# Optimization experiments

Hardware: AMD Instinct MI355X
Metric: run time of the kernel (lower is better)

The kernel has to match this reference:

```python
import jax, jax.numpy as jnp
import numpy as np

N_NODES = 50000
N_EDGES = 800000
DIM = 128
HEADS = 8
DK = DIM // HEADS  # 16
SQRT_DK = float(np.sqrt(DK))


def setup_inputs() -> dict:
    key = jax.random.key(0)
    ks = jax.random.split(key, 12)
    inp = {
        "h": jax.random.normal(ks[0], (N_NODES, DIM), jnp.float32),
        "src": jax.random.randint(ks[1], (N_EDGES,), 0, N_NODES, jnp.int32),
        "dst": jax.random.randint(ks[2], (N_EDGES,), 0, N_NODES, jnp.int32),
        "Wk": jax.random.normal(ks[3], (DIM, DIM), jnp.float32) / np.sqrt(DIM),
        "bk": jnp.zeros((DIM,), jnp.float32),
        "Wq": jax.random.normal(ks[4], (DIM, DIM), jnp.float32) / np.sqrt(DIM),
        "bq": jnp.zeros((DIM,), jnp.float32),
        "Wv": jax.random.normal(ks[5], (DIM, DIM), jnp.float32) / np.sqrt(DIM),
        "bv": jnp.zeros((DIM,), jnp.float32),
        "Wa": jax.random.normal(ks[6], (DIM, DIM), jnp.float32) / np.sqrt(DIM),
        "ba": jnp.zeros((DIM,), jnp.float32),
        "rel_att": jax.random.normal(ks[7], (HEADS, DK, DK), jnp.float32) / np.sqrt(DK),
        "rel_msg": jax.random.normal(ks[8], (HEADS, DK, DK), jnp.float32) / np.sqrt(DK),
        "rel_pri": jnp.ones((HEADS,), jnp.float32),
        "skip": jnp.ones((1,), jnp.float32),
    }
    return inp


def reference(h, src, dst, Wk, bk, Wq, bq, Wv, bv, Wa, ba, rel_att, rel_msg, rel_pri, skip):
    N = h.shape[0]
    # node-level projections -> [N, H, d_k]
    k = (h @ Wk + bk).reshape(N, HEADS, DK)
    q = (h @ Wq + bq).reshape(N, HEADS, DK)
    v = (h @ Wv + bv).reshape(N, HEADS, DK)
    # relation-specific transforms
    k = jnp.einsum('nhi,hij->nhj', k, rel_att)
    v = jnp.einsum('nhi,hij->nhj', v, rel_msg)
    # per-edge score: dot(q[dst], k[src]) over d_k -> [E, H]
    score = jnp.einsum('ehd,ehd->eh', q[dst], k[src]) * rel_pri / SQRT_DK
    # segment softmax over destination nodes (edge_softmax, norm_by='dst')
    smax = jax.ops.segment_max(score, dst, num_segments=N)  # [N, H]
    e = jnp.exp(score - smax[dst])
    ssum = jax.ops.segment_sum(e, dst, num_segments=N)  # [N, H]
    attn = e / ssum[dst]  # [E, H]
    # weighted scatter-sum of messages: sum_e v[src_e] * attn_e -> [N, H, d_k]
    m = v[src] * attn[:, :, None]
    t = jax.ops.segment_sum(m, dst, num_segments=N).reshape(N, DIM)
    # target-specific aggregation (dropout in eval mode = identity, use_norm=False)
    trans_out = t @ Wa + ba
    alpha = jax.nn.sigmoid(skip)  # [1], broadcasts
    new_h = trans_out * alpha + h * (1.0 - alpha)
    return new_h
```

## Files before the change

kernel.cpp:

```cpp
#include <hip/hip_runtime.h>
#include <stdint.h>

#define NN 50000
#define NE 800000

typedef __bf16 v8bf __attribute__((ext_vector_type(8)));
typedef float  v4f  __attribute__((ext_vector_type(4)));

#define EXP2F(x) __builtin_amdgcn_exp2f(x)

__device__ __forceinline__ float bf2f(unsigned short u) {
    return __uint_as_float(((unsigned)u) << 16);
}
__device__ __forceinline__ unsigned short f2bf(float f) {
    unsigned u = __float_as_uint(f);
    u += 0x7FFFu + ((u >> 16) & 1u);
    return (unsigned short)(u >> 16);
}
__device__ __forceinline__ float ldf(const void* p, size_t i, int isb) {
    return isb ? bf2f(((const unsigned short*)p)[i]) : ((const float*)p)[i];
}

__global__ __launch_bounds__(128) void k_prep(
    const void* __restrict__ Wq, const void* __restrict__ bq,
    const void* __restrict__ Wk, const void* __restrict__ bk,
    const void* __restrict__ Wv, const void* __restrict__ bv,
    const void* __restrict__ Wa, const void* __restrict__ ba,
    const void* __restrict__ rel_att, const void* __restrict__ rel_msg,
    const void* __restrict__ rel_pri,
    int* __restrict__ FLAG, unsigned short* __restrict__ WTb,
    float* __restrict__ BC, unsigned* __restrict__ CNT,
    unsigned* __restrict__ CUR, unsigned* __restrict__ DONE)
{
    const unsigned rp0 = ((const unsigned*)rel_pri)[0];
    const int isb = ((rp0 & 0xFFFFu) != 0u) ? 1 : 0;
    int b = blockIdx.x;
    int m = b >> 7;
    int i = b & 127;
    int j = threadIdx.x;
    int t = b * 128 + j;
    if (t < 50048) { CNT[t] = 0u; CUR[t] = 0u; }
    if (t == 0) { FLAG[0] = isb; DONE[0] = 0u; }
    if (m == 0) {
        WTb[((size_t)(0 * 128 + j)) * 128 + i] = f2bf(ldf(Wq, i * 128 + j, isb));
        if (i == 0) BC[j] = ldf(bq, j, isb);
    } else if (m == 3) {
        WTb[((size_t)(3 * 128 + j)) * 128 + i] = f2bf(ldf(Wa, i * 128 + j, isb));
        if (i == 0) BC[3 * 128 + j] = ldf(ba, j, isb);
    } else {
        const void* W    = (m == 1) ? Wk : Wv;
        const void* bias = (m == 1) ? bk : bv;
        const void* R    = (m == 1) ? rel_att : rel_msg;
        int hh = j >> 4, jj = j & 15;
        float scale = (m == 1) ? ldf(rel_pri, hh, isb) * 0.25f : 1.0f;
        float acc = 0.f, bacc = 0.f;
        #pragma unroll
        for (int l = 0; l < 16; ++l) {
            float r = ldf(R, hh * 256 + l * 16 + jj, isb);
            acc  += ldf(W, i * 128 + hh * 16 + l, isb) * r;
            bacc += ldf(bias, hh * 16 + l, isb) * r;
        }
        WTb[((size_t)(m * 128 + j)) * 128 + i] = f2bf(acc * scale);
        if (i == 0) BC[m * 128 + j] = bacc * scale;
    }
}

__global__ __launch_bounds__(256) void k_qkvh(
    const void* __restrict__ h, const unsigned short* __restrict__ WTb,
    const float* __restrict__ BC, const int* __restrict__ FLAG,
    const int* __restrict__ dst, unsigned* __restrict__ CNT,
    unsigned short* __restrict__ Qb, unsigned short* __restrict__ KVb)
{
    __shared__ __align__(16) unsigned short Ah[64][136];
    __shared__ __align__(16) unsigned short Bh[128][136];
    const int tid = threadIdx.x;

    if (blockIdx.x >= 782) {
        int e = (blockIdx.x - 782) * 256 + tid;
        atomicAdd(&CNT[dst[e]], 1u);
        return;
    }

    const int isb = FLAG[0];
    const int rowBase = blockIdx.x * 64;

    if (isb) {
        #pragma unroll
        for (int i = 0; i < 4; ++i) {
            int lin = tid + i * 256;
            int row = lin >> 4, kc = (lin & 15) * 8;
            int gr = rowBase + row;
            uint4 u = make_uint4(0, 0, 0, 0);
            if (gr < NN) u = *(const uint4*)((const unsigned short*)h + (size_t)gr * 128 + kc);
            *(uint4*)&Ah[row][kc] = u;
        }
    } else {
        #pragma unroll
        for (int i = 0; i < 8; ++i) {
            int lin = tid + i * 256;
            int row = lin >> 5, c4 = (lin & 31) * 4;
            int gr = rowBase + row;
            ushort4 o = make_ushort4(0, 0, 0, 0);
            if (gr < NN) {
                float4 f = *(const float4*)((const float*)h + (size_t)gr * 128 + c4);
                o.x = f2bf(f.x); o.y = f2bf(f.y); o.z = f2bf(f.z); o.w = f2bf(f.w);
            }
            *(ushort4*)&Ah[row][c4] = o;
        }
    }

    const int w = tid >> 6, l = tid & 63;
    const int lr = l & 15, q = l >> 4;

    for (int m = 0; m < 3; ++m) {
        if (m) __syncthreads();
        #pragma unroll
        for (int i = 0; i < 8; ++i) {
            int lin = tid + i * 256;
            int col = lin >> 4, kc = (lin & 15) * 8;
            uint4 u = *(const uint4*)(WTb + ((size_t)(m * 128 + col)) * 128 + kc);
            *(uint4*)&Bh[col][kc] = u;
        }
        __syncthreads();

        v4f acc[8];
        #pragma unroll
        for (int nt = 0; nt < 8; ++nt) {
            float bj = BC[m * 128 + nt * 16 + lr];
            acc[nt] = (v4f){bj, bj, bj, bj};
        }
        #pragma unroll
        for (int kk = 0; kk < 4; ++kk) {
            v8bf a = *(const v8bf*)&Ah[w * 16 + lr][kk * 32 + q * 8];
            #pragma unroll
            for (int nt = 0; nt < 8; ++nt) {
                v8bf b = *(const v8bf*)&Bh[nt * 16 + lr][kk * 32 + q * 8];
                acc[nt] = __builtin_amdgcn_mfma_f32_16x16x32_bf16(a, b, acc[nt], 0, 0, 0);
            }
        }
        #pragma unroll
        for (int nt = 0; nt < 8; ++nt) {
            #pragma unroll
            for (int r = 0; r < 4; ++r) {
                int row = rowBase + w * 16 + q * 4 + r;
                if (row < NN) {
                    int col = nt * 16 + lr;
                    unsigned short val = f2bf(acc[nt][r]);
                    if (m == 0) Qb[(size_t)row * 128 + col] = val;
                    else        KVb[(size_t)row * 256 + col * 2 + (m - 1)] = val;
                }
            }
        }
    }
}

#define SCB 512
#define NSB 98
__global__ __launch_bounds__(SCB) void k_scan(
    const unsigned* __restrict__ CNT, unsigned* __restrict__ RPS,
    unsigned* __restrict__ BSUM, unsigned* __restrict__ BOFF,
    unsigned* __restrict__ DONE)
{
    __shared__ unsigned sh[SCB];
    __shared__ int lastFlag;
    int tid = threadIdx.x;
    int g = blockIdx.x * SCB + tid;
    unsigned v = (g < NN) ? CNT[g] : 0u;
    sh[tid] = v;
    __syncthreads();
    #pragma unroll
    for (int off = 1; off < SCB; off <<= 1) {
        unsigned t = 0;
        if (tid >= off) t = sh[tid - off];
        __syncthreads();
        if (tid >= off) sh[tid] += t;
        __syncthreads();
    }
    if (g < NN) RPS[g] = sh[tid] - v;
    if (tid == SCB - 1) atomicExch(&BSUM[blockIdx.x], sh[tid]);
    __syncthreads();
    if (tid == 0) {
        __threadfence();
        lastFlag = (atomicAdd(DONE, 1u) == NSB - 1);
    }
    __syncthreads();
    if (!lastFlag) return;

    unsigned bv = (tid < NSB) ? atomicAdd(&BSUM[tid], 0u) : 0u;
    sh[tid] = bv;
    __syncthreads();
    #pragma unroll
    for (int off = 1; off < SCB; off <<= 1) {
        unsigned t = 0;
        if (tid >= off) t = sh[tid - off];
        __syncthreads();
        if (tid >= off) sh[tid] += t;
        __syncthreads();
    }
    if (tid < NSB) BOFF[tid] = sh[tid] - bv;
}

__global__ __launch_bounds__(256) void k_fill(
    const int* __restrict__ src, const int* __restrict__ dst,
    const unsigned* __restrict__ RPS, const unsigned* __restrict__ BOFF,
    unsigned* __restrict__ CUR, int* __restrict__ ESRC)
{
    int e = blockIdx.x * 256 + threadIdx.x;
    int d = dst[e];
    int pos = (int)atomicAdd(&CUR[d], 1u);
    ESRC[(int)(RPS[d] + BOFF[d >> 9]) + pos] = src[e];
}

__global__ __launch_bounds__(256) void k_attn(
    const unsigned* __restrict__ RPS, const unsigned* __restrict__ BOFF,
    const int* __restrict__ ESRC,
    const unsigned short* __restrict__ Qb, const unsigned short* __restrict__ KVb,
    unsigned short* __restrict__ Tb)
{
    int d = (blockIdx.x * 256 + threadIdx.x) >> 6;
    int lane = threadIdx.x & 63;
    int beg = (int)(RPS[d] + BOFF[d >> 9]);
    int end = (d == NN - 1) ? NE : (int)(RPS[d + 1] + BOFF[(d + 1) >> 9]);
    const float LOG2E = 1.4426950408889634f;

    ushort2 qq = *(const ushort2*)(Qb + (size_t)d * 128 + lane * 2);
    float q0 = bf2f(qq.x) * LOG2E, q1 = bf2f(qq.y) * LOG2E;

    float s = 0.f, o0 = 0.f, o1 = 0.f;
    int j = beg;
    for (; j + 8 <= end; j += 8) {
        ushort4 kv[8];
        #pragma unroll
        for (int t = 0; t < 8; ++t) {
            int sid = ESRC[j + t];
            kv[t] = *(const ushort4*)(KVb + (size_t)sid * 256 + lane * 4);
        }
        #pragma unroll
        for (int t = 0; t < 8; ++t) {
            float p = q0 * bf2f(kv[t].x) + q1 * bf2f(kv[t].z);
            p += __shfl_xor(p, 1);
            p += __shfl_xor(p, 2);
            p += __shfl_xor(p, 4);
            float w = EXP2F(p);
            s  += w;
            o0 += w * bf2f(kv[t].y);
            o1 += w * bf2f(kv[t].w);
        }
    }
    for (; j < end; ++j) {
        int sid = ESRC[j];
        ushort4 kv = *(const ushort4*)(KVb + (size_t)sid * 256 + lane * 4);
        float p = q0 * bf2f(kv.x) + q1 * bf2f(kv.z);
        p += __shfl_xor(p, 1);
        p += __shfl_xor(p, 2);
        p += __shfl_xor(p, 4);
        float w = EXP2F(p);
        s  += w;
        o0 += w * bf2f(kv.y);
        o1 += w * bf2f(kv.w);
    }
    float r = (s > 0.f) ? (1.0f / s) : 0.f;
    ushort2 o;
    o.x = f2bf(o0 * r); o.y = f2bf(o1 * r);
    *(ushort2*)(Tb + (size_t)d * 128 + lane * 2) = o;
}

__global__ __launch_bounds__(256) void k_final_m(
    const unsigned short* __restrict__ Tb, const unsigned short* __restrict__ WTb,
    const float* __restrict__ BC, const void* __restrict__ h,
    const void* __restrict__ skip, const int* __restrict__ FLAG,
    void* __restrict__ out)
{
    __shared__ __align__(16) unsigned short Ah[64][136];
    __shared__ __align__(16) unsigned short Bh[128][136];
    const int isb = FLAG[0];
    const int tid = threadIdx.x;
    const int rowBase = blockIdx.x * 64;

    #pragma unroll
    for (int i = 0; i < 4; ++i) {
        int lin = tid + i * 256;
        int row = lin >> 4, kc = (lin & 15) * 8;
        int gr = rowBase + row;
        uint4 u = make_uint4(0, 0, 0, 0);
        if (gr < NN) u = *(const uint4*)(Tb + (size_t)gr * 128 + kc);
        *(uint4*)&Ah[row][kc] = u;
    }
    #pragma unroll
    for (int i = 0; i < 8; ++i) {
        int lin = tid + i * 256;
        int col = lin >> 4, kc = (lin & 15) * 8;
        uint4 u = *(const uint4*)(WTb + ((size_t)(3 * 128 + col)) * 128 + kc);
        *(uint4*)&Bh[col][kc] = u;
    }
    __syncthreads();

    const int w = tid >> 6, l = tid & 63;
    const int lr = l & 15, q = l >> 4;
    v4f acc[8];
    #pragma unroll
    for (int nt = 0; nt < 8; ++nt) {
        float bj = BC[3 * 128 + nt * 16 + lr];
        acc[nt] = (v4f){bj, bj, bj, bj};
    }
    #pragma unroll
    for (int kk = 0; kk < 4; ++kk) {
        v8bf a = *(const v8bf*)&Ah[w * 16 + lr][kk * 32 + q * 8];
        #pragma unroll
        for (int nt = 0; nt < 8; ++nt) {
            v8bf b = *(const v8bf*)&Bh[nt * 16 + lr][kk * 32 + q * 8];
            acc[nt] = __builtin_amdgcn_mfma_f32_16x16x32_bf16(a, b, acc[nt], 0, 0, 0);
        }
    }
    float skipv = ldf(skip, 0, isb);
    float alpha = 1.0f / (1.0f + __expf(-skipv));
    float beta = 1.0f - alpha;
    #pragma unroll
    for (int nt = 0; nt < 8; ++nt) {
        #pragma unroll
        for (int r = 0; r < 4; ++r) {
            int row = rowBase + w * 16 + q * 4 + r;
            if (row < NN) {
                size_t off = (size_t)row * 128 + nt * 16 + lr;
                float hv = ldf(h, off, isb);
                float o = alpha * acc[nt][r] + beta * hv;
                if (isb) ((unsigned short*)out)[off] = f2bf(o);
                else     ((float*)out)[off] = o;
            }
        }
    }
}

extern "C" void kernel_launch(void* const* d_in, const int* in_sizes, int n_in,
                              void* d_out, int out_size, void* d_ws, size_t ws_size,
                              hipStream_t stream)
{
    const void* h  = d_in[0];
    const int* src = (const int*)d_in[1];
    const int* dst = (const int*)d_in[2];
    const void* Wk = d_in[3];
    const void* bk = d_in[4];
    const void* Wq = d_in[5];
    const void* bq = d_in[6];
    const void* Wv = d_in[7];
    const void* bv = d_in[8];
    const void* Wa = d_in[9];
    const void* ba = d_in[10];
    const void* rel_att = d_in[11];
    const void* rel_msg = d_in[12];
    const void* rel_pri = d_in[13];
    const void* skip    = d_in[14];

    float* F = (float*)d_ws;
    int* FLAG      = (int*)F;
    float* BC      = F + 16;
    unsigned short* WTb = (unsigned short*)(BC + 512);
    unsigned* CNT  = (unsigned*)((float*)(BC + 512) + 32768);
    unsigned* CUR  = CNT + 50048;
    unsigned* RPS  = CUR + 50048;
    unsigned* BSUM = RPS + 50048;
    unsigned* BOFF = BSUM + 128;
    unsigned* DONE = BOFF + 128;
    unsigned short* Tb = (unsigned short*)(DONE + 16);
    int* ESRC      = (int*)(Tb + (size_t)NN * 128);
    unsigned short* Qb  = (unsigned short*)(ESRC + NE);
    unsigned short* KVb = Qb + (size_t)NN * 128;

    k_prep<<<512, 128, 0, stream>>>(Wq, bq, Wk, bk, Wv, bv, Wa, ba,
                                    rel_att, rel_msg, rel_pri, FLAG, WTb, BC,
                                    CNT, CUR, DONE);
    k_qkvh<<<782 + 3125, 256, 0, stream>>>(h, WTb, BC, FLAG, dst, CNT, Qb, KVb);
    k_scan<<<NSB, SCB, 0, stream>>>(CNT, RPS, BSUM, BOFF, DONE);
    k_fill<<<NE / 256, 256, 0, stream>>>(src, dst, RPS, BOFF, CUR, ESRC);
    k_attn<<<(NN * 64) / 256, 256, 0, stream>>>(RPS, BOFF, ESRC, Qb, KVb, Tb);
    k_final_m<<<782, 256, 0, stream>>>(Tb, WTb, BC, h, skip, FLAG, d_out);
}
```

Baseline: 290.0 us.

## Move degree counting into prep, pair K/V stores, and pad attention loop

```diff
diff --git a/kernel.cpp b/kernel.cpp
--- a/kernel.cpp
+++ b/kernel.cpp
@@ -27,20 +27,23 @@
     const void* __restrict__ Wv, const void* __restrict__ bv,
     const void* __restrict__ Wa, const void* __restrict__ ba,
     const void* __restrict__ rel_att, const void* __restrict__ rel_msg,
-    const void* __restrict__ rel_pri,
+    const void* __restrict__ rel_pri, const int* __restrict__ dst,
+    unsigned* __restrict__ CNT,
     int* __restrict__ FLAG, unsigned short* __restrict__ WTb,
-    float* __restrict__ BC, unsigned* __restrict__ CNT,
-    unsigned* __restrict__ CUR, unsigned* __restrict__ DONE)
-{
+    float* __restrict__ BC)
+{
+    int b = blockIdx.x;
+    int j = threadIdx.x;
+    if (b >= 512) {
+        int e = (b - 512) * 128 + j;
+        atomicAdd(&CNT[dst[e]], 1u);
+        return;
+    }
     const unsigned rp0 = ((const unsigned*)rel_pri)[0];
     const int isb = ((rp0 & 0xFFFFu) != 0u) ? 1 : 0;
-    int b = blockIdx.x;
     int m = b >> 7;
     int i = b & 127;
-    int j = threadIdx.x;
-    int t = b * 128 + j;
-    if (t < 50048) { CNT[t] = 0u; CUR[t] = 0u; }
-    if (t == 0) { FLAG[0] = isb; DONE[0] = 0u; }
+    if (b == 0 && j == 0) FLAG[0] = isb;
     if (m == 0) {
         WTb[((size_t)(0 * 128 + j)) * 128 + i] = f2bf(ldf(Wq, i * 128 + j, isb));
         if (i == 0) BC[j] = ldf(bq, j, isb);
@@ -65,23 +68,15 @@
     }
 }
 
-__global__ __launch_bounds__(256) void k_qkvh(
+__global__ __launch_bounds__(256) void k_qkv(
     const void* __restrict__ h, const unsigned short* __restrict__ WTb,
     const float* __restrict__ BC, const int* __restrict__ FLAG,
-    const int* __restrict__ dst, unsigned* __restrict__ CNT,
     unsigned short* __restrict__ Qb, unsigned short* __restrict__ KVb)
 {
     __shared__ __align__(16) unsigned short Ah[64][136];
     __shared__ __align__(16) unsigned short Bh[128][136];
+    const int isb = FLAG[0];
     const int tid = threadIdx.x;
-
-    if (blockIdx.x >= 782) {
-        int e = (blockIdx.x - 782) * 256 + tid;
-        atomicAdd(&CNT[dst[e]], 1u);
-        return;
-    }
-
-    const int isb = FLAG[0];
     const int rowBase = blockIdx.x * 64;
 
     if (isb) {
@@ -111,6 +106,7 @@
 
     const int w = tid >> 6, l = tid & 63;
     const int lr = l & 15, q = l >> 4;
+    v4f accK[8];
 
     for (int m = 0; m < 3; ++m) {
         if (m) __syncthreads();
@@ -138,18 +134,31 @@
                 acc[nt] = __builtin_amdgcn_mfma_f32_16x16x32_bf16(a, b, acc[nt], 0, 0, 0);
             }
         }
-        #pragma unroll
-        for (int nt = 0; nt < 8; ++nt) {
+        if (m == 0) {
             #pragma unroll
-            for (int r = 0; r < 4; ++r) {
-                int row = rowBase + w * 16 + q * 4 + r;
-                if (row < NN) {
-                    int col = nt * 16 + lr;
-                    unsigned short val = f2bf(acc[nt][r]);
-                    if (m == 0) Qb[(size_t)row * 128 + col] = val;
-                    else        KVb[(size_t)row * 256 + col * 2 + (m - 1)] = val;
+            for (int nt = 0; nt < 8; ++nt)
+                #pragma unroll
+                for (int r = 0; r < 4; ++r) {
+                    int row = rowBase + w * 16 + q * 4 + r;
+                    if (row < NN)
+                        Qb[(size_t)row * 128 + nt * 16 + lr] = f2bf(acc[nt][r]);
                 }
-            }
+        } else if (m == 1) {
+            #pragma unroll
+            for (int nt = 0; nt < 8; ++nt) accK[nt] = acc[nt];
+        } else {
+            #pragma unroll
+            for (int nt = 0; nt < 8; ++nt)
+                #pragma unroll
+                for (int r = 0; r < 4; ++r) {
+                    int row = rowBase + w * 16 + q * 4 + r;
+                    if (row < NN) {
+                        ushort2 kv;
+                        kv.x = f2bf(accK[nt][r]);
+                        kv.y = f2bf(acc[nt][r]);
+                        *(ushort2*)&KVb[(size_t)row * 256 + (nt * 16 + lr) * 2] = kv;
+                    }
+                }
         }
     }
 }
@@ -159,12 +168,13 @@
 __global__ __launch_bounds__(SCB) void k_scan(
     const unsigned* __restrict__ CNT, unsigned* __restrict__ RPS,
     unsigned* __restrict__ BSUM, unsigned* __restrict__ BOFF,
-    unsigned* __restrict__ DONE)
+    unsigned* __restrict__ DONE, unsigned* __restrict__ CUR)
 {
     __shared__ unsigned sh[SCB];
     __shared__ int lastFlag;
     int tid = threadIdx.x;
     int g = blockIdx.x * SCB + tid;
+    if (g < 50048) CUR[g] = 0u;
     unsigned v = (g < NN) ? CNT[g] : 0u;
     sh[tid] = v;
     __syncthreads();
@@ -227,12 +237,12 @@
     float q0 = bf2f(qq.x) * LOG2E, q1 = bf2f(qq.y) * LOG2E;
 
     float s = 0.f, o0 = 0.f, o1 = 0.f;
-    int j = beg;
-    for (; j + 8 <= end; j += 8) {
+    for (int j = beg; j < end; j += 8) {
         ushort4 kv[8];
         #pragma unroll
         for (int t = 0; t < 8; ++t) {
-            int sid = ESRC[j + t];
+            int idx = j + t;
+            int sid = ESRC[(idx < end) ? idx : (end - 1)];
             kv[t] = *(const ushort4*)(KVb + (size_t)sid * 256 + lane * 4);
         }
         #pragma unroll
@@ -241,23 +251,11 @@
             p += __shfl_xor(p, 1);
             p += __shfl_xor(p, 2);
             p += __shfl_xor(p, 4);
-            float w = EXP2F(p);
+            float w = (j + t < end) ? EXP2F(p) : 0.f;
             s  += w;
             o0 += w * bf2f(kv[t].y);
             o1 += w * bf2f(kv[t].w);
         }
-    }
-    for (; j < end; ++j) {
-        int sid = ESRC[j];
-        ushort4 kv = *(const ushort4*)(KVb + (size_t)sid * 256 + lane * 4);
-        float p = q0 * bf2f(kv.x) + q1 * bf2f(kv.z);
-        p += __shfl_xor(p, 1);
-        p += __shfl_xor(p, 2);
-        p += __shfl_xor(p, 4);
-        float w = EXP2F(p);
-        s  += w;
-        o0 += w * bf2f(kv.y);
-        o1 += w * bf2f(kv.w);
     }
     float r = (s > 0.f) ? (1.0f / s) : 0.f;
     ushort2 o;
@@ -356,21 +354,23 @@
     float* BC      = F + 16;
     unsigned short* WTb = (unsigned short*)(BC + 512);
     unsigned* CNT  = (unsigned*)((float*)(BC + 512) + 32768);
-    unsigned* CUR  = CNT + 50048;
+    unsigned* DONE = CNT + 50048;
+    unsigned* CUR  = DONE + 16;
     unsigned* RPS  = CUR + 50048;
     unsigned* BSUM = RPS + 50048;
     unsigned* BOFF = BSUM + 128;
-    unsigned* DONE = BOFF + 128;
-    unsigned short* Tb = (unsigned short*)(DONE + 16);
+    unsigned short* Tb = (unsigned short*)(BOFF + 128);
     int* ESRC      = (int*)(Tb + (size_t)NN * 128);
     unsigned short* Qb  = (unsigned short*)(ESRC + NE);
     unsigned short* KVb = Qb + (size_t)NN * 128;
 
-    k_prep<<<512, 128, 0, stream>>>(Wq, bq, Wk, bk, Wv, bv, Wa, ba,
-                                    rel_att, rel_msg, rel_pri, FLAG, WTb, BC,
-                                    CNT, CUR, DONE);
-    k_qkvh<<<782 + 3125, 256, 0, stream>>>(h, WTb, BC, FLAG, dst, CNT, Qb, KVb);
-    k_scan<<<NSB, SCB, 0, stream>>>(CNT, RPS, BSUM, BOFF, DONE);
+    (void)hipMemsetAsync(CNT, 0, (50048 + 16) * sizeof(unsigned), stream);
+
+    k_prep<<<512 + 6250, 128, 0, stream>>>(Wq, bq, Wk, bk, Wv, bv, Wa, ba,
+                                           rel_att, rel_msg, rel_pri, dst, CNT,
+                                           FLAG, WTb, BC);
+    k_qkv<<<782, 256, 0, stream>>>(h, WTb, BC, FLAG, Qb, KVb);
+    k_scan<<<NSB, SCB, 0, stream>>>(CNT, RPS, BSUM, BOFF, DONE, CUR);
     k_fill<<<NE / 256, 256, 0, stream>>>(src, dst, RPS, BOFF, CUR, ESRC);
     k_attn<<<(NN * 64) / 256, 256, 0, stream>>>(RPS, BOFF, ESRC, Qb, KVb, Tb);
     k_final_m<<<782, 256, 0, stream>>>(Tb, WTb, BC, h, skip, FLAG, d_out);
```

Measured after the change: 285.6 us. About the same (-1.5%).
